# Kernel tuning notes

Hardware: AMD Instinct MI355X
Metric: run time of the kernel (lower is better)

The kernel has to match this reference:

```python
import jax, jax.numpy as jnp
import numpy as np


def _box_iou(a, b):
    # a: [K,4], b: [K,4] in ltrb; returns [K,K] pairwise IoU (torchvision box_iou math)
    area_a = jnp.clip(a[:, 2] - a[:, 0], 0) * jnp.clip(a[:, 3] - a[:, 1], 0)
    area_b = jnp.clip(b[:, 2] - b[:, 0], 0) * jnp.clip(b[:, 3] - b[:, 1], 0)
    lt = jnp.maximum(a[:, None, :2], b[None, :, :2])
    rb = jnp.minimum(a[:, None, 2:], b[None, :, 2:])
    wh = jnp.clip(rb - lt, 0)
    inter = wh[..., 0] * wh[..., 1]
    return inter / (area_a[:, None] + area_b[None, :] - inter + 1e-9)


def _nms_class(score, boxes, th_c, nms_th, K):
    # score: [N], boxes: [N,4]. Keep boxes with score > th_c, take top-K by score,
    # then greedy NMS suppressing lower-scored boxes with IoU >= nms_th (original keeps iou < nms_th).
    masked = jnp.where(score > th_c, score, -jnp.inf)
    top_s, idx = jax.lax.top_k(masked, K)          # descending score order
    valid = top_s > -jnp.inf
    bk = boxes[idx]                                 # [K,4]
    iou = _box_iou(bk, bk)                          # [K,K]
    order = jnp.arange(K)

    def body(alive, i):
        keep_i = alive[i]
        suppress = keep_i & (iou[i] >= nms_th) & (order > i)
        return alive & ~suppress, keep_i

    _, keep = jax.lax.scan(body, valid, order)
    return jnp.where(keep[:, None], bk, 0.0), jnp.where(keep, top_s, 0.0), keep


def decode(bboxes_in, scores_in, dboxes_xywh, conf_th, nms_th, max_num, scale_xy, scale_wh):
    B, C = bboxes_in.shape[0], scores_in.shape[1]
    K = int(max_num)
    # scale_back_batch: xywh offsets -> ltrb absolute boxes, softmax over classes
    b = jnp.transpose(bboxes_in, (0, 2, 1))                         # [B,N,4]
    xy = scale_xy * b[..., :2] * dboxes_xywh[..., 2:] + dboxes_xywh[..., :2]
    wh = jnp.exp(scale_wh * b[..., 2:]) * dboxes_xywh[..., 2:]
    ltrb = jnp.concatenate([xy - 0.5 * wh, xy + 0.5 * wh], axis=-1)  # [B,N,4]
    probs = jax.nn.softmax(jnp.transpose(scores_in, (0, 2, 1)), axis=-1)  # [B,N,C]
    cls_scores = jnp.transpose(probs[..., 1:], (0, 2, 1))            # [B,C-1,N] (skip background cls 0)

    def per_image(scores_cn, boxes_n4):
        f = jax.vmap(lambda s, t: _nms_class(s, boxes_n4, t, nms_th, K))
        return f(scores_cn, conf_th)

    bk, sk, keep = jax.vmap(per_image)(cls_scores, ltrb)  # [B,C-1,K,4], [B,C-1,K], [B,C-1,K]
    M = (C - 1) * K
    labels = jnp.arange(1, C, dtype=jnp.float32)[None, :, None] * keep.astype(jnp.float32)
    return (bk.reshape(B, M, 4), labels.reshape(B, M), sk.reshape(B, M), keep.reshape(B, M))


def setup_inputs() -> dict:
    key = jax.random.key(0)
    k0, k1, k2, k3, k4 = jax.random.split(key, 5)
    B, N, C = 32, 24564, 21
    bboxes_in = 0.5 * jax.random.normal(k0, (B, 4, N), jnp.float32)
    scores_in = jax.random.normal(k1, (B, C, N), jnp.float32)
    cxy = jax.random.uniform(k2, (1, N, 2), jnp.float32)
    dwh = jax.random.uniform(k3, (1, N, 2), jnp.float32, 0.05, 0.5)
    dboxes_xywh = jnp.concatenate([cxy, dwh], axis=-1)
    conf_th = jax.random.uniform(k4, (C - 1,), jnp.float32, 0.01, 0.05)
    return {
        'bboxes_in': bboxes_in,
        'scores_in': scores_in,
        'dboxes_xywh': dboxes_xywh,
        'conf_th': conf_th,
        'nms_th': jnp.float32(0.5),
        'max_num': 200,
        'scale_xy': 0.1,
        'scale_wh': 0.2,
    }


def reference(bboxes_in, scores_in, dboxes_xywh, conf_th, nms_th, max_num, scale_xy, scale_wh):
    # Padded, jit-compatible equivalent of the torch Decoder: per image we return
    # [(C-1)*K] slots of (boxes, labels, scores) with a boolean keep-mask; the torch
    # version returns only the kept (variable-length) entries, in the same order.
    return decode(bboxes_in, scores_in, dboxes_xywh, conf_th, nms_th, max_num, scale_xy, scale_wh)
```

## Files before the change

### kernel.cpp

```cpp
#include <hip/hip_runtime.h>
#include <math.h>

typedef unsigned int uint;
typedef unsigned short u16;
typedef unsigned long long u64;

#define NT 256
#define KTOP 200
#define CAP 256
#define CAPC 3072
#define SEGS 4
#define SEGCAP 512
#define NCLS 21
#define C1 20
#define MROWS 208
#define NSPLIT 48

struct Rec { float4 box; double lse; double pad; };

__device__ __forceinline__ u64 flip64(double d) {
  u64 u = (u64)__double_as_longlong(d);
  return (u & 0x8000000000000000ULL) ? ~u : (u | 0x8000000000000000ULL);
}

__device__ __forceinline__ double unflip64(u64 k) {
  u64 u = (k & 0x8000000000000000ULL) ? (k ^ 0x8000000000000000ULL) : ~k;
  return __longlong_as_double((long long)u);
}

__device__ __forceinline__ uint q_key16(float sf) {
  float qf = (sf + 16.0f) * 4096.0f;
  qf = fmaxf(fminf(qf, 65535.0f), 1.0f);
  return (uint)qf;
}

__device__ __forceinline__ void wave_walk(const uint* hist, uint* res,
                                          uint rank, int tid) {
  if (tid < 64) {
    int lane = tid;
    uint4 h = reinterpret_cast<const uint4*>(hist)[lane];
    uint s = h.x + h.y + h.z + h.w;
    uint suf = s;
#pragma unroll
    for (int off = 1; off < 64; off <<= 1) {
      uint o = (uint)__shfl_down((int)suf, off);
      if (lane + off < 64) suf += o;
    }
    uint sn = (uint)__shfl_down((int)suf, 1);
    if (lane == 63) sn = 0;
    uint c3 = h.w + sn, c2 = c3 + h.z, c1 = c2 + h.y, c0 = c1 + h.x;
    u64 m = __ballot(suf >= rank);
    int l = (m != 0) ? (63 - __clzll(m)) : 0;
    uint b3 = (uint)__shfl((int)c3, l);
    uint b2 = (uint)__shfl((int)c2, l);
    uint b1 = (uint)__shfl((int)c1, l);
    uint b0 = (uint)__shfl((int)c0, l);
    uint hx = (uint)__shfl((int)h.x, l);
    uint hy = (uint)__shfl((int)h.y, l);
    uint hz = (uint)__shfl((int)h.z, l);
    uint hw = (uint)__shfl((int)h.w, l);
    if (lane == 0) {
      uint binoff, S, hb;
      if (b3 >= rank)      { binoff = 3; S = b3; hb = hw; }
      else if (b2 >= rank) { binoff = 2; S = b2; hb = hz; }
      else if (b1 >= rank) { binoff = 1; S = b1; hb = hy; }
      else                 { binoff = 0; S = b0; hb = hx; }
      res[0] = (uint)(4 * l + (int)binoff);
      res[1] = S;
      res[2] = hb;
    }
  }
}

__global__ __launch_bounds__(NT) void zero_ghist(uint* __restrict__ g) {
  g[(size_t)blockIdx.x * NT + threadIdx.x] = 0;
}

__global__ __launch_bounds__(NT) void prep_kernel(
    const float* __restrict__ bboxes, const float* __restrict__ scores,
    const float* __restrict__ dboxes, const float* __restrict__ conf_th,
    const float* __restrict__ scale_xy_p, const float* __restrict__ scale_wh_p,
    Rec* __restrict__ recs, u16* __restrict__ keys_out,
    uint* __restrict__ ghist,
    int B, int N, int npad, int perblk)
{
  __shared__ double s_logth[C1];
  __shared__ uint lhist[C1 * 256];
  int tid = threadIdx.x;
  if (tid < C1) s_logth[tid] = log((double)conf_th[tid]);
  for (int i = tid; i < C1 * 256; i += NT) lhist[i] = 0;
  __syncthreads();

  int b = blockIdx.x / NSPLIT, j = blockIdx.x - b * NSPLIT;
  int s0 = j * perblk, e0 = min(N, s0 + perblk);
  int half = (e0 - s0) >> 1;
  float sxy = *scale_xy_p, swh = *scale_wh_p;

  for (int p = tid; p < half; p += NT) {
    int n = s0 + 2 * p;
    const float* bb = bboxes + (size_t)b * 4 * N + n;
    float2 bx = *reinterpret_cast<const float2*>(bb);
    float2 by = *reinterpret_cast<const float2*>(bb + (size_t)N);
    float2 bw = *reinterpret_cast<const float2*>(bb + 2 * (size_t)N);
    float2 bh = *reinterpret_cast<const float2*>(bb + 3 * (size_t)N);
    float4 d0 = reinterpret_cast<const float4*>(dboxes)[n];
    float4 d1 = reinterpret_cast<const float4*>(dboxes)[n + 1];
    float x0 = sxy * bx.x * d0.z + d0.x;
    float y0 = sxy * by.x * d0.w + d0.y;
    float w0 = expf(swh * bw.x) * d0.z;
    float h0 = expf(swh * bh.x) * d0.w;
    float x1 = sxy * bx.y * d1.z + d1.x;
    float y1 = sxy * by.y * d1.w + d1.y;
    float w1 = expf(swh * bw.y) * d1.z;
    float h1 = expf(swh * bh.y) * d1.w;

    const float* sc = scores + (size_t)b * NCLS * N + n;
    float2 v[NCLS];
    float mx0 = -INFINITY, mx1 = -INFINITY;
#pragma unroll
    for (int c = 0; c < NCLS; ++c) {
      float2 t = *reinterpret_cast<const float2*>(sc + (size_t)c * N);
      v[c] = t;
      mx0 = fmaxf(mx0, t.x);
      mx1 = fmaxf(mx1, t.y);
    }
    double a0 = 0.0, a1 = 0.0, a2 = 0.0;
    double b0 = 0.0, b1 = 0.0, b2 = 0.0;
#pragma unroll
    for (int c = 0; c < NCLS; ++c) {
      float e0f = __expf(v[c].x - mx0);
      float e1f = __expf(v[c].y - mx1);
      if ((c % 3) == 0)      { a0 += (double)e0f; b0 += (double)e1f; }
      else if ((c % 3) == 1) { a1 += (double)e0f; b1 += (double)e1f; }
      else                   { a2 += (double)e0f; b2 += (double)e1f; }
    }
    double lse0 = (double)mx0 + log(a0 + a1 + a2);
    double lse1 = (double)mx1 + log(b0 + b1 + b2);

    int gid = b * N + n;
    Rec r0, r1;
    r0.box = make_float4(x0 - 0.5f * w0, y0 - 0.5f * h0, x0 + 0.5f * w0, y0 + 0.5f * h0);
    r0.lse = lse0; r0.pad = 0.0;
    r1.box = make_float4(x1 - 0.5f * w1, y1 - 0.5f * h1, x1 + 0.5f * w1, y1 + 0.5f * h1);
    r1.lse = lse1; r1.pad = 0.0;
    recs[gid] = r0;
    recs[gid + 1] = r1;

#pragma unroll
    for (int c = 0; c < C1; ++c) {
      double s0d = (double)v[c + 1].x - lse0;
      double s1d = (double)v[c + 1].y - lse1;
      uint k0 = 0, k1 = 0;
      if (s0d > s_logth[c]) k0 = q_key16((float)s0d);
      if (s1d > s_logth[c]) k1 = q_key16((float)s1d);
      *reinterpret_cast<uint*>(keys_out + ((size_t)b * C1 + c) * npad + n)
          = k0 | (k1 << 16);
      if (k0) atomicAdd(&lhist[c * 256 + (k0 >> 8)], 1u);
      if (k1) atomicAdd(&lhist[c * 256 + (k1 >> 8)], 1u);
    }
  }
  if (j == NSPLIT - 1 && npad > N) {
    int pad = npad - N;
    for (int t = tid; t < pad * C1; t += NT) {
      int c = t / pad, n = N + (t - c * pad);
      keys_out[((size_t)b * C1 + c) * npad + n] = 0;
    }
  }
  __syncthreads();
  for (int i = tid; i < C1 * 256; i += NT) {
    uint v2 = lhist[i];
    if (v2) atomicAdd(&ghist[((size_t)b * C1 + (i >> 8)) * 256 + (i & 255)], v2);
  }
}

__global__ __launch_bounds__(NT) void collect_kernel(
    const u16* __restrict__ keys, const uint* __restrict__ ghist,
    uint4* __restrict__ L0cnt, uint* __restrict__ cand, uint* __restrict__ cnts,
    int npad)
{
  int blk = blockIdx.x;
  int task = blk >> 2, seg = blk & (SEGS - 1);
  int tid = threadIdx.x, lane = tid & 63;
  __shared__ uint sL, sCnt0, sCnt;

  if (tid < 64) {
    uint4 h = reinterpret_cast<const uint4*>(ghist + (size_t)task * 256)[tid];
    uint s = h.x + h.y + h.z + h.w;
    uint suf = s;
#pragma unroll
    for (int off = 1; off < 64; off <<= 1) {
      uint o = (uint)__shfl_down((int)suf, off);
      if (lane + off < 64) suf += o;
    }
    uint total = (uint)__shfl((int)suf, 0);
    uint sn = (uint)__shfl_down((int)suf, 1);
    if (lane == 63) sn = 0;
    uint c3 = h.w + sn, c2 = c3 + h.z, c1 = c2 + h.y, c0 = c1 + h.x;
    uint binoff, cnt, abv;
    if (c3 >= KTOP)      { binoff = 3; cnt = c3; abv = c3 - h.w; }
    else if (c2 >= KTOP) { binoff = 2; cnt = c2; abv = c2 - h.z; }
    else if (c1 >= KTOP) { binoff = 1; cnt = c1; abv = c1 - h.y; }
    else                 { binoff = 0; cnt = c0; abv = c0 - h.x; }
    uint L0v, cnt0v, abovev;
    if (total < KTOP) {
      L0v = 1u; cnt0v = total; abovev = 0u;
    } else {
      u64 m = __ballot(suf >= KTOP);
      int l = 63 - __clzll(m);
      uint bo = (uint)__shfl((int)binoff, l);
      cnt0v = (uint)__shfl((int)cnt, l);
      abovev = (uint)__shfl((int)abv, l);
      L0v = ((uint)(4 * l) + bo) << 8;
    }
    if (lane == 0) {
      sL = L0v; sCnt0 = cnt0v;
      if (seg == 0) L0cnt[task] = make_uint4(L0v, cnt0v, abovev, total);
    }
  }
  if (tid == NT - 1) sCnt = 0;
  __syncthreads();

  uint L = sL, cnt0 = sCnt0;
  if (cnt0 > CAPC) { if (tid == 0) cnts[blk] = 0; return; }

  const u16* krow = keys + (size_t)task * npad;
  const uint4* krow8 = reinterpret_cast<const uint4*>(krow);
  int nv8 = npad >> 3;
  int per8 = (nv8 + SEGS - 1) >> 2;
  int s8 = seg * per8, e8 = min(nv8, s8 + per8);
  uint* myc = cand + ((size_t)task * SEGS + seg) * SEGCAP;

  for (int i = s8 + tid; i < e8; i += NT) {
    uint4 kv = krow8[i];
    uint base = (uint)(i << 3);
    uint ks[8] = { kv.x & 0xFFFFu, kv.x >> 16, kv.y & 0xFFFFu, kv.y >> 16,
                   kv.z & 0xFFFFu, kv.z >> 16, kv.w & 0xFFFFu, kv.w >> 16 };
#pragma unroll
    for (int comp = 0; comp < 8; ++comp) {
      uint k = ks[comp];
      bool f = (k >= L);
      u64 m = __ballot(f);
      if (m) {
        uint nb = (uint)__popcll(m);
        uint wb = 0;
        if (lane == 0) wb = atomicAdd(&sCnt, nb);
        wb = (uint)__shfl((int)wb, 0);
        if (f) {
          uint pos = wb + (uint)__popcll(m & ((1ULL << lane) - 1ULL));
          if (pos < SEGCAP) myc[pos] = (k << 15) | (base + comp);
        }
      }
    }
  }
  __syncthreads();
  if (tid == 0) cnts[blk] = sCnt;
}

__global__ __launch_bounds__(NT) void final_kernel(
    const u16* __restrict__ keys, const uint4* __restrict__ L0cnt,
    const uint* __restrict__ candg, const uint* __restrict__ cnts,
    const float* __restrict__ scores, const Rec* __restrict__ recs,
    const float* __restrict__ nms_th_p,
    float* __restrict__ out, int B, int N, int npad)
{
  int task = blockIdx.x;
  int b = task / C1, c = task - b * C1;
  int tid = threadIdx.x, lane = tid & 63, wav = tid >> 6;
  const u16* krow = keys + (size_t)task * npad;
  int nv8 = npad >> 3;

  __shared__ uint cand[CAPC];
  __shared__ uint histB[256];
  __shared__ uint res3[4];
  __shared__ uint scq[SEGS];
  __shared__ int si[CAP];
  __shared__ u64 sC[CAP];
  __shared__ u64 skid[CAP];
  __shared__ float4 sbx[CAP];
  __shared__ float4 sbox[MROWS];
  __shared__ float sar[MROWS];
  __shared__ u64 smaskT[13][64];
  __shared__ u64 saliveW[4];
  __shared__ uint sCnt, sCnt2;

  uint4 w0 = L0cnt[task];
  uint cnt0 = w0.y;
  if (tid < SEGS) scq[tid] = cnts[task * SEGS + tid];
  if (tid == 0) { sCnt = 0; sCnt2 = 0; }
  if (tid < MROWS) { sbox[tid] = make_float4(0.f, 0.f, 0.f, 0.f); sar[tid] = 0.f; }
  __syncthreads();
  bool slow = (cnt0 > CAPC) ||
              (scq[0] > SEGCAP) || (scq[1] > SEGCAP) ||
              (scq[2] > SEGCAP) || (scq[3] > SEGCAP);

  uint pref = w0.x >> 8, above = w0.z, rank = KTOP - w0.z;
  uint cnt;

  if (!slow) {
    uint off1 = scq[0], off2 = off1 + scq[1], off3 = off2 + scq[2];
    cnt = off3 + scq[3];
    const uint* cg = candg + (size_t)task * SEGS * SEGCAP;
    for (int j = tid; j < (int)scq[0]; j += NT) cand[j] = cg[j];
    for (int j = tid; j < (int)scq[1]; j += NT) cand[off1 + j] = cg[SEGCAP + j];
    for (int j = tid; j < (int)scq[2]; j += NT) cand[off2 + j] = cg[2 * SEGCAP + j];
    for (int j = tid; j < (int)scq[3]; j += NT) cand[off3 + j] = cg[3 * SEGCAP + j];
    __syncthreads();
  } else {
    const uint4* krow8 = reinterpret_cast<const uint4*>(krow);
    histB[tid] = 0;
    __syncthreads();
    for (int i = tid; i < nv8; i += NT) {
      uint4 kv = krow8[i];
      uint ks[8] = { kv.x & 0xFFFFu, kv.x >> 16, kv.y & 0xFFFFu, kv.y >> 16,
                     kv.z & 0xFFFFu, kv.z >> 16, kv.w & 0xFFFFu, kv.w >> 16 };
#pragma unroll
      for (int comp = 0; comp < 8; ++comp) {
        uint k = ks[comp];
        if ((k >> 8) == pref) atomicAdd(&histB[k & 255u], 1u);
      }
    }
    __syncthreads();
    wave_walk(histB, res3, rank, tid);
    __syncthreads();
    uint Ts = (pref << 8) | res3[0];
    for (int i = tid; i < nv8; i += NT) {
      uint4 kv = krow8[i];
      uint base = (uint)(i << 3);
      uint ks[8] = { kv.x & 0xFFFFu, kv.x >> 16, kv.y & 0xFFFFu, kv.y >> 16,
                     kv.z & 0xFFFFu, kv.z >> 16, kv.w & 0xFFFFu, kv.w >> 16 };
#pragma unroll
      for (int comp = 0; comp < 8; ++comp) {
        uint k = ks[comp];
        bool f = (k >= Ts);
        u64 m = __ballot(f);
        if (m) {
          uint nb = (uint)__popcll(m);
          uint wb = 0;
          if (lane == 0) wb = atomicAdd(&sCnt, nb);
          wb = (uint)__shfl((int)wb, 0);
          if (f) {
            uint pos = wb + (uint)__popcll(m & ((1ULL << lane) - 1ULL));
            if (pos < CAPC) cand[pos] = (k << 15) | (base + comp);
          }
        }
      }
    }
    __syncthreads();
    cnt = min(sCnt, (uint)CAPC);
  }

  uint cntF;
  if (cnt <= CAP) {
    for (int p = tid; p < (int)cnt; p += NT) si[p] = (int)(cand[p] & 0x7FFFu);
    __syncthreads();
    cntF = cnt;
  } else {
    histB[tid] = 0;
    __syncthreads();
    for (int p = tid; p < (int)cnt; p += NT) {
      uint k = cand[p] >> 15;
      if ((k >> 8) == pref) atomicAdd(&histB[k & 255u], 1u);
    }
    __syncthreads();
    wave_walk(histB, res3, rank, tid);
    __syncthreads();
    uint T = (pref << 8) | res3[0];
    for (int p = tid; p < (int)cnt; p += NT) {
      uint cd = cand[p];
      if ((cd >> 15) >= T) {
        uint q = atomicAdd(&sCnt2, 1u);
        if (q < CAP) si[q] = (int)(cd & 0x7FFFu);
      }
    }
    __syncthreads();
    cntF = min(sCnt2, (uint)CAP);
  }

  int valid_cnt = (int)min(cntF, (uint)KTOP);

  {
    int p = tid;
    u64 C;
    if (p < (int)cntF) {
      int n = si[p];
      const Rec* rc = recs + (size_t)b * N + n;
      float4 box = rc->box;
      double l = rc->lse;
      double s = (double)scores[((size_t)b * NCLS + (c + 1)) * N + n] - l;
      u64 f = flip64(s);
      C = (f & ~0x7FFFULL) | (u64)(32767 - n);
      sbx[p] = box;
    } else {
      C = (u64)p;
      sbx[p] = make_float4(0.f, 0.f, 0.f, 0.f);
    }
    sC[p] = C;
  }
  __syncthreads();

  {
    u64 kp = sC[tid];
    int r = 0;
#pragma unroll 8
    for (int jj = 0; jj < CAP; ++jj) r += (sC[jj] > kp) ? 1 : 0;
    if (tid < (int)cntF && r < KTOP) {
      skid[r] = kp;
      float4 bx = sbx[tid];
      sbox[r] = bx;
      sar[r] = fmaxf(bx.z - bx.x, 0.f) * fmaxf(bx.w - bx.y, 0.f);
    }
  }
  __syncthreads();

  float nth = *nms_th_p;

  {
    float4 jb0 = sbox[lane], jb1 = sbox[lane + 64], jb2 = sbox[lane + 128];
    float4 jb3 = (lane + 192 < MROWS) ? sbox[lane + 192]
                                      : make_float4(0.f, 0.f, 0.f, 0.f);
    float ja0 = sar[lane], ja1 = sar[lane + 64], ja2 = sar[lane + 128],
          ja3 = (lane + 192 < MROWS) ? sar[lane + 192] : 0.f;
    for (int w = wav; w < 13; w += 4) {
      u64 word = 0;
      int r0 = w * 16;
#pragma unroll
      for (int rr = 0; rr < 16; ++rr) {
        int r = r0 + rr;
        float4 rb = sbox[r];
        float ra = sar[r];
        uint nib = 0;
#define IOU_BIT(K, JB, JA) { \
        int j = lane + 64 * (K); \
        float xx1 = fmaxf(rb.x, JB.x), yy1 = fmaxf(rb.y, JB.y); \
        float xx2 = fminf(rb.z, JB.z), yy2 = fminf(rb.w, JB.w); \
        float ww = fmaxf(xx2 - xx1, 0.f), hh = fmaxf(yy2 - yy1, 0.f); \
        float inter = ww * hh; \
        float den = ((ra + JA) - inter) + 1e-9f; \
        if ((inter >= nth * den) && (j > r)) nib |= 1u << (K); }
        IOU_BIT(0, jb0, ja0) IOU_BIT(1, jb1, ja1)
        IOU_BIT(2, jb2, ja2) IOU_BIT(3, jb3, ja3)
#undef IOU_BIT
        word |= (u64)nib << (rr * 4);
      }
      smaskT[w][lane] = word;
    }
  }
  __syncthreads();

  if (tid < 64) {
    u64 mm[13];
#pragma unroll
    for (int w = 0; w < 13; ++w) mm[w] = smaskT[w][lane];
    uint av = 0;
#pragma unroll
    for (int k = 0; k < 4; ++k)
      if (lane + 64 * k < valid_cnt) av |= 1u << k;
#define STEP(i) { \
    u64 bm = __ballot((lane == ((i) & 63)) && ((av >> ((i) >> 6)) & 1u)); \
    if (bm) av &= ~((uint)((mm[(i) >> 4] >> (((i) & 15) * 4)) & 0xFULL)); }
#define S4(i)  STEP(i) STEP((i)+1) STEP((i)+2) STEP((i)+3)
#define S16(i) S4(i) S4((i)+4) S4((i)+8) S4((i)+12)
#define S64(i) S16(i) S16((i)+16) S16((i)+32) S16((i)+48)
    S64(0) S64(64) S64(128) S16(192)
#undef S64
#undef S16
#undef S4
#undef STEP
#pragma unroll
    for (int k = 0; k < 4; ++k) {
      u64 bb2 = __ballot((av >> k) & 1u);
      if (lane == 0) saliveW[k] = bb2;
    }
  }
  __syncthreads();

  size_t M = (size_t)C1 * KTOP;
  float* out_boxes  = out;
  float* out_labels = out + (size_t)B * M * 4;
  float* out_scores = out_labels + (size_t)B * M;
  float* out_keep   = out_scores + (size_t)B * M;
  if (tid < KTOP) {
    size_t slot = ((size_t)b * C1 + c) * KTOP + tid;
    bool kept = (tid < valid_cnt) && ((saliveW[tid >> 6] >> (tid & 63)) & 1ULL);
    float4 bx = kept ? sbox[tid] : make_float4(0.f, 0.f, 0.f, 0.f);
    reinterpret_cast<float4*>(out_boxes)[slot] = bx;
    out_labels[slot] = kept ? (float)(c + 1) : 0.0f;
    out_scores[slot] = kept ? (float)exp(unflip64(skid[tid])) : 0.0f;
    out_keep[slot]   = kept ? 1.0f : 0.0f;
  }
}

extern "C" void kernel_launch(void* const* d_in, const int* in_sizes, int n_in,
                              void* d_out, int out_size, void* d_ws, size_t ws_size,
                              hipStream_t stream) {
  const float* bboxes   = (const float*)d_in[0];
  const float* scores   = (const float*)d_in[1];
  const float* dboxes   = (const float*)d_in[2];
  const float* conf_th  = (const float*)d_in[3];
  const float* nms_th   = (const float*)d_in[4];
  const float* scale_xy = (const float*)d_in[6];
  const float* scale_wh = (const float*)d_in[7];

  int N = in_sizes[2] / 4;
  int B = in_sizes[0] / (4 * N);
  int npad = (N + 7) & ~7;

  char* ws = (char*)d_ws;
  size_t off = 0;
  Rec*    recs    = (Rec*)   (ws + off); off += (size_t)B * N * sizeof(Rec);
  u16*    keys    = (u16*)   (ws + off); off += (size_t)B * C1 * npad * 2;
  uint*   ghist   = (uint*)  (ws + off); off += (size_t)B * C1 * 256 * 4;
  uint4*  L0cnt   = (uint4*) (ws + off); off += (size_t)B * C1 * 16;
  uint*   cand    = (uint*)  (ws + off); off += (size_t)B * C1 * SEGS * SEGCAP * 4;
  uint*   cnts    = (uint*)  (ws + off);

  zero_ghist<<<B * C1, NT, 0, stream>>>(ghist);

  int perblk = ((N + NSPLIT - 1) / NSPLIT + 1) & ~1;
  prep_kernel<<<B * NSPLIT, NT, 0, stream>>>(
      bboxes, scores, dboxes, conf_th, scale_xy, scale_wh,
      recs, keys, ghist, B, N, npad, perblk);

  collect_kernel<<<B * C1 * SEGS, NT, 0, stream>>>(
      keys, ghist, L0cnt, cand, cnts, npad);

  final_kernel<<<B * C1, NT, 0, stream>>>(
      keys, L0cnt, cand, cnts, scores, recs, nms_th,
      (float*)d_out, B, N, npad);
}
```

Before: 92.54 us.

## Replace precomputed IoU mask matrix with on-the-fly greedy NMS in one wave

The old code had all four waves build a full 208x208 IoU suppression bitmask in shared memory, then one wave ran a fully unrolled greedy scan over it. The new code drops the mask and has a single wave walk candidates in order. It computes IoU only for rows that are still alive and clears suppressed bits at once. This skips IoU work for suppressed rows, a barrier and the shared mask, but it serialises all IoU arithmetic onto one wave and uses a data-dependent loop instead of an unrolled scan.

```diff
diff --git a/kernel.cpp b/kernel.cpp
--- a/kernel.cpp
+++ b/kernel.cpp
@@ -265,7 +265,7 @@
 {
   int task = blockIdx.x;
   int b = task / C1, c = task - b * C1;
-  int tid = threadIdx.x, lane = tid & 63, wav = tid >> 6;
+  int tid = threadIdx.x, lane = tid & 63;
   const u16* krow = keys + (size_t)task * npad;
   int nv8 = npad >> 3;
 
@@ -279,7 +279,6 @@
   __shared__ float4 sbx[CAP];
   __shared__ float4 sbox[MROWS];
   __shared__ float sar[MROWS];
-  __shared__ u64 smaskT[13][64];
   __shared__ u64 saliveW[4];
   __shared__ uint sCnt, sCnt2;
 
@@ -414,58 +413,35 @@
 
   float nth = *nms_th_p;
 
-  {
+  if (tid < 64) {
     float4 jb0 = sbox[lane], jb1 = sbox[lane + 64], jb2 = sbox[lane + 128];
     float4 jb3 = (lane + 192 < MROWS) ? sbox[lane + 192]
                                       : make_float4(0.f, 0.f, 0.f, 0.f);
     float ja0 = sar[lane], ja1 = sar[lane + 64], ja2 = sar[lane + 128],
           ja3 = (lane + 192 < MROWS) ? sar[lane + 192] : 0.f;
-    for (int w = wav; w < 13; w += 4) {
-      u64 word = 0;
-      int r0 = w * 16;
-#pragma unroll
-      for (int rr = 0; rr < 16; ++rr) {
-        int r = r0 + rr;
-        float4 rb = sbox[r];
-        float ra = sar[r];
-        uint nib = 0;
-#define IOU_BIT(K, JB, JA) { \
+    uint av = 0;
+#pragma unroll
+    for (int k = 0; k < 4; ++k)
+      if (lane + 64 * k < valid_cnt) av |= 1u << k;
+
+    for (int i = 0; i < valid_cnt; ++i) {
+      u64 bm = __ballot((lane == (i & 63)) && ((av >> (i >> 6)) & 1u));
+      if (bm) {
+        float4 rb = sbox[i];
+        float ra = sar[i];
+#define IOU_KILL(K, JB, JA) { \
         int j = lane + 64 * (K); \
         float xx1 = fmaxf(rb.x, JB.x), yy1 = fmaxf(rb.y, JB.y); \
         float xx2 = fminf(rb.z, JB.z), yy2 = fminf(rb.w, JB.w); \
         float ww = fmaxf(xx2 - xx1, 0.f), hh = fmaxf(yy2 - yy1, 0.f); \
         float inter = ww * hh; \
         float den = ((ra + JA) - inter) + 1e-9f; \
-        if ((inter >= nth * den) && (j > r)) nib |= 1u << (K); }
-        IOU_BIT(0, jb0, ja0) IOU_BIT(1, jb1, ja1)
-        IOU_BIT(2, jb2, ja2) IOU_BIT(3, jb3, ja3)
-#undef IOU_BIT
-        word |= (u64)nib << (rr * 4);
+        if ((inter >= nth * den) && (j > i)) av &= ~(1u << (K)); }
+        IOU_KILL(0, jb0, ja0) IOU_KILL(1, jb1, ja1)
+        IOU_KILL(2, jb2, ja2) IOU_KILL(3, jb3, ja3)
+#undef IOU_KILL
       }
-      smaskT[w][lane] = word;
-    }
-  }
-  __syncthreads();
-
-  if (tid < 64) {
-    u64 mm[13];
-#pragma unroll
-    for (int w = 0; w < 13; ++w) mm[w] = smaskT[w][lane];
-    uint av = 0;
-#pragma unroll
-    for (int k = 0; k < 4; ++k)
-      if (lane + 64 * k < valid_cnt) av |= 1u << k;
-#define STEP(i) { \
-    u64 bm = __ballot((lane == ((i) & 63)) && ((av >> ((i) >> 6)) & 1u)); \
-    if (bm) av &= ~((uint)((mm[(i) >> 4] >> (((i) & 15) * 4)) & 0xFULL)); }
-#define S4(i)  STEP(i) STEP((i)+1) STEP((i)+2) STEP((i)+3)
-#define S16(i) S4(i) S4((i)+4) S4((i)+8) S4((i)+12)
-#define S64(i) S16(i) S16((i)+16) S16((i)+32) S16((i)+48)
-    S64(0) S64(64) S64(128) S16(192)
-#undef S64
-#undef S16
-#undef S4
-#undef STEP
+    }
 #pragma unroll
     for (int k = 0; k < 4; ++k) {
       u64 bb2 = __ballot((av >> k) & 1u);
```

After: 109.2 us. 1.18x slower.
